# Kernel tuning notes

Hardware: AMD Instinct MI355X
Metric: run time of the kernel (lower is better)

## Reference

```python
import jax, jax.numpy as jnp
import numpy as np

B, N, C, H = 2, 2048, 1024, 16
D = C // H  # head_dim = 64
EPS = 1e-6


def _rope_freqs(n, d):
    inv_freq = 1.0 / (10000.0 ** (np.arange(0, d // 2, dtype=np.float32) * 2.0 / d))
    ang = np.arange(n, dtype=np.float32)[:, None] * inv_freq[None, :]  # [N, D/2]
    ang = np.concatenate([ang, ang], axis=-1)  # [N, D] (chunk-in-half convention)
    cos = jnp.asarray(np.cos(ang))[None, None]  # [1,1,N,D]
    sin = jnp.asarray(np.sin(ang))[None, None]
    return cos, sin


def setup_inputs() -> dict:
    key = jax.random.key(0)
    k1, k2, k3 = jax.random.split(key, 3)
    x = jax.random.normal(k1, (B, N, C), dtype=jnp.float32)
    w_qkv = jax.random.normal(k2, (3 * C, C), dtype=jnp.float32) * (C ** -0.5)
    w_proj = jax.random.normal(k3, (C, C), dtype=jnp.float32) * (C ** -0.5)
    b_proj = jnp.zeros((C,), dtype=jnp.float32)
    freqs_cos, freqs_sin = _rope_freqs(N, D)
    return {"x": x, "w_qkv": w_qkv, "w_proj": w_proj, "b_proj": b_proj,
            "freqs_cos": freqs_cos, "freqs_sin": freqs_sin}


def _layernorm(t):
    # affine-free LayerNorm over the last (head_dim) axis
    mu = jnp.mean(t, axis=-1, keepdims=True)
    var = jnp.var(t, axis=-1, keepdims=True)
    return (t - mu) * jax.lax.rsqrt(var + EPS)


def _rotate_half(t):
    t1, t2 = jnp.split(t, 2, axis=-1)
    return jnp.concatenate([-t2, t1], axis=-1)


def reference(x, w_qkv, w_proj, b_proj, freqs_cos, freqs_sin):
    b, n, c = x.shape
    qkv = jnp.einsum('bnc,kc->bnk', x, w_qkv)  # [B,N,3C]
    qkv = qkv.reshape(b, n, 3, H, D).transpose(2, 0, 3, 1, 4)  # [3,B,H,N,D]
    q, k, v = qkv[0], qkv[1], qkv[2]
    q = _layernorm(q)
    k = _layernorm(k)
    q = q * freqs_cos + _rotate_half(q) * freqs_sin
    k = k * freqs_cos + _rotate_half(k) * freqs_sin
    scale = D ** -0.5
    scores = jnp.einsum('bhqd,bhkd->bhqk', q, k) * scale  # [B,H,N,N]
    attn = jax.nn.softmax(scores, axis=-1)
    out = jnp.einsum('bhqk,bhkd->bhqd', attn, v)  # [B,H,N,D]
    out = out.transpose(0, 2, 1, 3).reshape(b, n, c)
    return jnp.einsum('bnc,oc->bno', out, w_proj) + b_proj
```

## Files before the change

### kernel.cpp

```cpp
#include <hip/hip_runtime.h>
#include <hip/hip_bf16.h>


typedef __bf16 bf16x8 __attribute__((ext_vector_type(8)));
typedef float f32x4 __attribute__((ext_vector_type(4)));
typedef float f32x16 __attribute__((ext_vector_type(16)));
typedef unsigned short us8 __attribute__((ext_vector_type(8)));
typedef unsigned short us4 __attribute__((ext_vector_type(4)));

static __device__ __forceinline__ unsigned short f2b(float f) {
  __hip_bfloat16 h = __float2bfloat16(f);
  return __builtin_bit_cast(unsigned short, h);
}
static __device__ __forceinline__ float b2f(unsigned short u) {
  __hip_bfloat16 h = __builtin_bit_cast(__hip_bfloat16, u);
  return __bfloat162float(h);
}

#if __has_builtin(__builtin_amdgcn_exp2f)
static __device__ __forceinline__ float fast_exp2(float x) { return __builtin_amdgcn_exp2f(x); }
#else
static __device__ __forceinline__ float fast_exp2(float x) { return exp2f(x); }
#endif

static __device__ __forceinline__ void async_copy16(void* lds, const void* g) {
  __builtin_amdgcn_global_load_lds(
      (const __attribute__((address_space(1))) void*)g,
      (__attribute__((address_space(3))) void*)lds, 16, 0, 0);
}

static __device__ __forceinline__ unsigned cvt_pk_bf16(float lo, float hi) {
  unsigned r;
  asm("v_cvt_pk_bf16_f32 %0, %1, %2" : "=v"(r) : "v"(lo), "v"(hi));
  return r;
}
static __device__ __forceinline__ void swap32(unsigned& x, unsigned& y) {
  asm("v_permlane32_swap_b32 %0, %1" : "+v"(x), "+v"(y));
}
static __device__ __forceinline__ float max3f(float a, float b, float c) {
  float d;
  asm("v_max3_f32 %0, %1, %2, %3" : "=v"(d) : "v"(a), "v"(b), "v"(c));
  return d;
}
static __device__ __forceinline__ float vmax16(const f32x16& v) {
  float a = max3f(v[0], v[1], v[2]);
  float b = max3f(v[3], v[4], v[5]);
  float c = max3f(v[6], v[7], v[8]);
  float d = max3f(v[9], v[10], v[11]);
  float e = max3f(v[12], v[13], v[14]);
  float x = max3f(a, b, c);
  float y = max3f(d, e, v[15]);
  return fmaxf(x, y);
}

__global__ __launch_bounds__(256) void cvt_bf16(
    const float* __restrict__ in, unsigned short* __restrict__ out, int n8) {
  int i = blockIdx.x * 256 + threadIdx.x;
  if (i >= n8) return;
  const float4* p = reinterpret_cast<const float4*>(in) + (size_t)i * 2;
  float4 a = p[0], b = p[1];
  us8 v;
  v[0] = f2b(a.x); v[1] = f2b(a.y); v[2] = f2b(a.z); v[3] = f2b(a.w);
  v[4] = f2b(b.x); v[5] = f2b(b.y); v[6] = f2b(b.z); v[7] = f2b(b.w);
  reinterpret_cast<us8*>(out)[i] = v;
}

__global__ __launch_bounds__(256, 2) void gemm_qkv(
    const unsigned short* __restrict__ A,
    const unsigned short* __restrict__ Bw,
    const float* __restrict__ fcos, const float* __restrict__ fsin,
    unsigned short* __restrict__ qo, unsigned short* __restrict__ ko,
    unsigned short* __restrict__ vt)
{
  __shared__ unsigned short a_sh[128 * 64];
  __shared__ unsigned short b_sh[128 * 64];
  const int tid = threadIdx.x;
  const int lane = tid & 63;
  const int w = tid >> 6;
  const int wr = w >> 1, wc = w & 1;
  const int l15 = lane & 15, l4 = lane >> 4;
  const int m0 = blockIdx.y * 128;
  const int n0 = blockIdx.x * 128;
  const int r8 = lane >> 3, c8 = lane & 7;
  const int K = 1024;

  f32x4 acc[4][4] = {};

  for (int k0 = 0; k0 < K; k0 += 64) {
#pragma unroll
    for (int p = 0; p < 8; ++p) {
      int s = p * 4 + w;
      if (s < 16) {
        int row = s * 8 + r8;
        async_copy16(&a_sh[s * 512],
                     &A[(size_t)(m0 + row) * K + k0 + ((c8 ^ (row & 7)) << 3)]);
      } else {
        int s2 = s - 16;
        int row = s2 * 8 + r8;
        async_copy16(&b_sh[s2 * 512],
                     &Bw[(size_t)(n0 + row) * K + k0 + ((c8 ^ (row & 7)) << 3)]);
      }
    }
    __syncthreads();
#pragma unroll
    for (int kk = 0; kk < 2; ++kk) {
      bf16x8 af[4], bfr[4];
#pragma unroll
      for (int mf = 0; mf < 4; ++mf) {
        int r = wr * 64 + mf * 16 + l15;
        af[mf] = *reinterpret_cast<const bf16x8*>(
            &a_sh[r * 64 + (((kk * 4 + l4) ^ (r & 7)) << 3)]);
      }
#pragma unroll
      for (int nf = 0; nf < 4; ++nf) {
        int r = wc * 64 + nf * 16 + l15;
        bfr[nf] = *reinterpret_cast<const bf16x8*>(
            &b_sh[r * 64 + (((kk * 4 + l4) ^ (r & 7)) << 3)]);
      }
#pragma unroll
      for (int mf = 0; mf < 4; ++mf)
#pragma unroll
        for (int nf = 0; nf < 4; ++nf)
          acc[mf][nf] = __builtin_amdgcn_mfma_f32_16x16x32_bf16(af[mf], bfr[nf], acc[mf][nf], 0, 0, 0);
    }
    __syncthreads();
  }

  const int colbase = n0 + wc * 64;
  const int three = colbase >> 10;
  const int hh = (colbase >> 6) & 15;
  const int b_ = m0 >> 11;
  const int nbase = (m0 & 2047) + wr * 64;
  unsigned short* ep = ((w < 2) ? a_sh : b_sh) + (w & 1) * 4096;
  const int cch = lane & 7, rb2 = lane >> 3;

  if (three < 2) {
    const float sc = three ? 1.f : 0.18033688011112042f;
#pragma unroll
    for (int mf = 0; mf < 4; ++mf) {
#pragma unroll
      for (int j = 0; j < 4; ++j) {
        float a0 = acc[mf][0][j], a1 = acc[mf][1][j];
        float a2 = acc[mf][2][j], a3 = acc[mf][3][j];
        float s1 = (a0 + a1) + (a2 + a3);
        float s2 = (a0 * a0 + a1 * a1) + (a2 * a2 + a3 * a3);
#pragma unroll
        for (int off = 8; off; off >>= 1) {
          s1 += __shfl_xor(s1, off);
          s2 += __shfl_xor(s2, off);
        }
        float mu = s1 * (1.f / 64.f);
        float inv = rsqrtf(s2 * (1.f / 64.f) - mu * mu + 1e-6f);
        int rloc = mf * 16 + l4 * 4 + j;
        int n = nbase + rloc;
        const float* cp = &fcos[(size_t)n * 64];
        const float* sp = &fsin[(size_t)n * 64];
#pragma unroll
        for (int nf = 0; nf < 4; ++nf) {
          int d = nf * 16 + l15;
          float tt = (acc[mf][nf][j] - mu) * inv;
          float tp = (acc[mf][nf ^ 2][j] - mu) * inv;
          float r = sc * (tt * cp[d] + ((nf < 2) ? -tp : tp) * sp[d]);
          ep[rloc * 64 + ((((d >> 3) ^ (rloc & 7)) << 3) | (d & 7))] = f2b(r);
        }
      }
    }
    unsigned short* dst =
        (three ? ko : qo) + (size_t)(b_ * 16 + hh) * 2048 * 64;
#pragma unroll
    for (int i = 0; i < 8; ++i) {
      int row = i * 8 + rb2;
      us8 vd = *reinterpret_cast<const us8*>(
          &ep[row * 64 + ((cch ^ (row & 7)) << 3)]);
      *reinterpret_cast<us8*>(&dst[(size_t)(nbase + row) * 64 + cch * 8]) = vd;
    }
  } else {
#pragma unroll
    for (int mf = 0; mf < 4; ++mf)
#pragma unroll
      for (int nf = 0; nf < 4; ++nf) {
        int d = nf * 16 + l15;
#pragma unroll
        for (int j = 0; j < 4; ++j) {
          int nl = mf * 16 + l4 * 4 + j;
          ep[d * 64 + ((((nl >> 3) ^ (d & 7)) << 3) | (nl & 7))] =
              f2b(acc[mf][nf][j]);
        }
      }
    unsigned short* dst = vt + (size_t)(b_ * 16 + hh) * 64 * 2048;
#pragma unroll
    for (int i = 0; i < 8; ++i) {
      int d = i * 8 + rb2;
      us8 vd = *reinterpret_cast<const us8*>(
          &ep[d * 64 + ((cch ^ (d & 7)) << 3)]);
      *reinterpret_cast<us8*>(&dst[(size_t)d * 2048 + nbase + cch * 8]) = vd;
    }
  }
}

__global__ __launch_bounds__(256, 2) void gemm_proj(
    const unsigned short* __restrict__ A, const unsigned short* __restrict__ Bw,
    const float* __restrict__ bias, float* __restrict__ Cout,
    int M, int Nn, int K) {
  __shared__ unsigned short a_sh[128 * 64];
  __shared__ unsigned short b_sh[128 * 64];
  const int tid = threadIdx.x;
  const int lane = tid & 63;
  const int w = tid >> 6;
  const int wr = w >> 1, wc = w & 1;
  const int l15 = lane & 15, l4 = lane >> 4;
  const int m0 = blockIdx.y * 128;
  const int n0 = blockIdx.x * 128;
  const int r8 = lane >> 3, c8 = lane & 7;

  f32x4 acc[4][4] = {};

  for (int k0 = 0; k0 < K; k0 += 64) {
#pragma unroll
    for (int p = 0; p < 8; ++p) {
      int s = p * 4 + w;
      if (s < 16) {
        int row = s * 8 + r8;
        async_copy16(&a_sh[s * 512],
                     &A[(size_t)(m0 + row) * K + k0 + ((c8 ^ (row & 7)) << 3)]);
      } else {
        int s2 = s - 16;
        int row = s2 * 8 + r8;
        async_copy16(&b_sh[s2 * 512],
                     &Bw[(size_t)(n0 + row) * K + k0 + ((c8 ^ (row & 7)) << 3)]);
      }
    }
    __syncthreads();
#pragma unroll
    for (int kk = 0; kk < 2; ++kk) {
      bf16x8 af[4], bfr[4];
#pragma unroll
      for (int mf = 0; mf < 4; ++mf) {
        int r = wr * 64 + mf * 16 + l15;
        af[mf] = *reinterpret_cast<const bf16x8*>(
            &a_sh[r * 64 + (((kk * 4 + l4) ^ (r & 7)) << 3)]);
      }
#pragma unroll
      for (int nf = 0; nf < 4; ++nf) {
        int r = wc * 64 + nf * 16 + l15;
        bfr[nf] = *reinterpret_cast<const bf16x8*>(
            &b_sh[r * 64 + (((kk * 4 + l4) ^ (r & 7)) << 3)]);
      }
#pragma unroll
      for (int mf = 0; mf < 4; ++mf)
#pragma unroll
        for (int nf = 0; nf < 4; ++nf)
          acc[mf][nf] = __builtin_amdgcn_mfma_f32_16x16x32_bf16(af[mf], bfr[nf], acc[mf][nf], 0, 0, 0);
    }
    __syncthreads();
  }
#pragma unroll
  for (int mf = 0; mf < 4; ++mf)
#pragma unroll
    for (int nf = 0; nf < 4; ++nf) {
      int col = n0 + wc * 64 + nf * 16 + l15;
#pragma unroll
      for (int j = 0; j < 4; ++j) {
        int row = m0 + wr * 64 + mf * 16 + l4 * 4 + j;
        Cout[(size_t)row * Nn + col] = acc[mf][nf][j] + bias[col];
      }
    }
}

__global__ __launch_bounds__(256, 4) void attn_kern(
    const unsigned short* __restrict__ Q,
    const unsigned short* __restrict__ Kk,
    const unsigned short* __restrict__ Vt,
    unsigned short* __restrict__ po,
    float* __restrict__ stats)
{
  __shared__ unsigned short k_sh[2][64 * 64];
  __shared__ unsigned short v_sh[2][64 * 64];
  const int tid = threadIdx.x;
  const int lane = tid & 63;
  const int w = tid >> 6;
  const int l31 = lane & 31;
  const int H = lane >> 5;
  const int bid = blockIdx.x;
  const int wid = (bid & 7) * 128 + (bid >> 3);
  const int split = wid & 1;
  const int qt = (wid >> 1) & 15;
  const int bh = wid >> 5;
  const int h = bh & 15, b = bh >> 4;
  const unsigned short* qb = Q + (size_t)bh * 2048 * 64;
  const unsigned short* kb = Kk + (size_t)bh * 2048 * 64;
  const unsigned short* vb = Vt + (size_t)bh * 64 * 2048;
  const int tok = qt * 128 + w * 32 + l31;
  const int kt0 = split * 16;

  bf16x8 qf[4];
#pragma unroll
  for (int c = 0; c < 4; ++c)
    qf[c] = *reinterpret_cast<const bf16x8*>(&qb[(size_t)tok * 64 + c * 16 + H * 8]);

  f32x16 oT[2] = {};
  float mr = -1e30f, lr = 0.f;

  const int r8 = lane >> 3, cc8 = lane & 7;
#define ATTN_STAGE(KT, BUF)                                                        \
  {                                                                                \
    _Pragma("unroll") for (int p = 0; p < 4; ++p) {                                \
      int sseg = p * 4 + w;                                                        \
      if (sseg < 8) {                                                              \
        int row = sseg * 8 + r8;                                                   \
        async_copy16(&k_sh[BUF][sseg * 512],                                       \
                     &kb[(size_t)((KT) * 64 + row) * 64 + ((cc8 ^ (row & 7)) << 3)]); \
      } else {                                                                     \
        int row = (sseg - 8) * 8 + r8;                                             \
        async_copy16(&v_sh[BUF][(sseg - 8) * 512],                                 \
                     &vb[(size_t)row * 2048 + (KT) * 64 + ((cc8 ^ (row & 7)) << 3)]); \
      }                                                                            \
    }                                                                              \
  }

  ATTN_STAGE(kt0, 0);
  __syncthreads();

  for (int kt = 0; kt < 16; ++kt) {
    const int cur = kt & 1;
    if (kt < 15) ATTN_STAGE(kt0 + kt + 1, cur ^ 1);

    f32x16 sT[2] = {};
#pragma unroll
    for (int c = 0; c < 4; ++c) {
      int ch0 = 2 * c + H;
#pragma unroll
      for (int t = 0; t < 2; ++t) {
        int r = t * 32 + l31;
        bf16x8 ka = *reinterpret_cast<const bf16x8*>(
            &k_sh[cur][r * 64 + ((ch0 ^ (r & 7)) << 3)]);
        sT[t] = __builtin_amdgcn_mfma_f32_32x32x16_bf16(ka, qf[c], sT[t], 0, 0, 0);
      }
    }
    float tmax = fmaxf(vmax16(sT[0]), vmax16(sT[1]));
    tmax = fmaxf(tmax, __shfl_xor(tmax, 32));
    if (__any(tmax > mr + 8.f)) {
      float mn = fmaxf(mr, tmax);
      float corr = fast_exp2(mr - mn);
      mr = mn;
      lr *= corr;
#pragma unroll
      for (int r = 0; r < 16; ++r) { oT[0][r] *= corr; oT[1][r] *= corr; }
    }
    float tsum = 0.f;
#pragma unroll
    for (int t = 0; t < 2; ++t)
#pragma unroll
      for (int r = 0; r < 16; ++r) {
        float p = fast_exp2(sT[t][r] - mr);
        sT[t][r] = p;
        tsum += p;
      }
    tsum += __shfl_xor(tsum, 32);
    lr += tsum;

    bf16x8 pB[4];
#pragma unroll
    for (int t = 0; t < 2; ++t)
#pragma unroll
      for (int half = 0; half < 2; ++half) {
        const int base = 8 * half;
        unsigned x0 = cvt_pk_bf16(sT[t][base + 0], sT[t][base + 1]);
        unsigned x1 = cvt_pk_bf16(sT[t][base + 2], sT[t][base + 3]);
        unsigned y0 = cvt_pk_bf16(sT[t][base + 4], sT[t][base + 5]);
        unsigned y1 = cvt_pk_bf16(sT[t][base + 6], sT[t][base + 7]);
        swap32(x0, y0);
        swap32(x1, y1);
        int4 packed = {(int)x0, (int)x1, (int)y0, (int)y1};
        pB[2 * t + half] = __builtin_bit_cast(bf16x8, packed);
      }
#pragma unroll
    for (int dt = 0; dt < 2; ++dt) {
      int r = dt * 32 + l31;
#pragma unroll
      for (int mi = 0; mi < 4; ++mi) {
        int ch = (mi * 2 + H) ^ (r & 7);
        bf16x8 va = *reinterpret_cast<const bf16x8*>(&v_sh[cur][r * 64 + (ch << 3)]);
        oT[dt] = __builtin_amdgcn_mfma_f32_32x32x16_bf16(va, pB[mi], oT[dt], 0, 0, 0);
      }
    }
    __syncthreads();
  }
  if (H == 0) {
    float2 st = {mr, lr};
    *reinterpret_cast<float2*>(
        &stats[(((size_t)split * 32 + bh) * 2048 + tok) * 2]) = st;
  }
  unsigned short* pd = po + (size_t)split * 4096 * 1024;
#pragma unroll
  for (int dt = 0; dt < 2; ++dt)
#pragma unroll
    for (int rb = 0; rb < 4; ++rb) {
      us4 ov;
#pragma unroll
      for (int j = 0; j < 4; ++j) ov[j] = f2b(oT[dt][rb * 4 + j]);
      *reinterpret_cast<us4*>(
          &pd[((size_t)b * 2048 + tok) * 1024 + h * 64 + 32 * dt + 8 * rb + 4 * H]) = ov;
    }
#undef ATTN_STAGE
}

__global__ __launch_bounds__(256) void attn_merge(
    const unsigned short* __restrict__ po,
    const float* __restrict__ stats,
    unsigned short* __restrict__ ao)
{
  int i = blockIdx.x * 256 + threadIdx.x;
  int row = i >> 8;
  int c4 = (i & 255) << 2;
  int b = row >> 11, tok = row & 2047, h = c4 >> 6;
  int bh = b * 16 + h;
  float2 s0 = *reinterpret_cast<const float2*>(&stats[((size_t)bh * 2048 + tok) * 2]);
  float2 s1 = *reinterpret_cast<const float2*>(
      &stats[(((size_t)32 + bh) * 2048 + tok) * 2]);
  float M = fmaxf(s0.x, s1.x);
  float w0 = fast_exp2(s0.x - M), w1 = fast_exp2(s1.x - M);
  float inv = 1.f / (s0.y * w0 + s1.y * w1);
  w0 *= inv; w1 *= inv;
  us4 a = *reinterpret_cast<const us4*>(&po[(size_t)i * 4]);
  us4 c = *reinterpret_cast<const us4*>(&po[(size_t)4096 * 1024 + i * 4]);
  us4 o;
#pragma unroll
  for (int j = 0; j < 4; ++j) o[j] = f2b(b2f(a[j]) * w0 + b2f(c[j]) * w1);
  *reinterpret_cast<us4*>(&ao[(size_t)i * 4]) = o;
}

extern "C" void kernel_launch(void* const* d_in, const int* in_sizes, int n_in,
                              void* d_out, int out_size, void* d_ws, size_t ws_size,
                              hipStream_t stream) {
  (void)in_sizes; (void)n_in; (void)out_size; (void)ws_size;
  const float* x      = (const float*)d_in[0];
  const float* w_qkv  = (const float*)d_in[1];
  const float* w_proj = (const float*)d_in[2];
  const float* b_proj = (const float*)d_in[3];
  const float* fcos   = (const float*)d_in[4];
  const float* fsin   = (const float*)d_in[5];
  float* out = (float*)d_out;
  char* ws = (char*)d_ws;

  unsigned short* x_bf     = (unsigned short*)(ws + 0);
  unsigned short* wqkv_bf  = (unsigned short*)(ws + 8388608);
  unsigned short* wproj_bf = (unsigned short*)(ws + 14680064);
  unsigned short* q_bf     = (unsigned short*)(ws + 16777216);
  unsigned short* k_bf     = (unsigned short*)(ws + 25165824);
  unsigned short* vt_bf    = (unsigned short*)(ws + 33554432);
  unsigned short* ao_bf    = (unsigned short*)(ws + 41943040);
  unsigned short* po_bf    = (unsigned short*)(ws + 50331648);
  float*          st_f     = (float*)(ws + 67108864);

  cvt_bf16<<<2048, 256, 0, stream>>>(x, x_bf, 4096 * 1024 / 8);
  cvt_bf16<<<1536, 256, 0, stream>>>(w_qkv, wqkv_bf, 3072 * 1024 / 8);
  cvt_bf16<<<512, 256, 0, stream>>>(w_proj, wproj_bf, 1024 * 1024 / 8);
  gemm_qkv<<<dim3(24, 32), 256, 0, stream>>>(x_bf, wqkv_bf, fcos, fsin,
                                             q_bf, k_bf, vt_bf);
  attn_kern<<<1024, 256, 0, stream>>>(q_bf, k_bf, vt_bf, po_bf, st_f);
  attn_merge<<<4096, 256, 0, stream>>>(po_bf, st_f, ao_bf);
  gemm_proj<<<dim3(8, 32), 256, 0, stream>>>(ao_bf, wproj_bf, b_proj, out,
                                             4096, 1024, 1024);
}
```

Baseline: 129.1 us.

## Drop split-KV attention and merge kernel, fuse bf16 conversions into one launch

```diff
diff --git a/kernel.cpp b/kernel.cpp
--- a/kernel.cpp
+++ b/kernel.cpp
@@ -53,19 +53,30 @@
   return fmaxf(x, y);
 }
 
-__global__ __launch_bounds__(256) void cvt_bf16(
-    const float* __restrict__ in, unsigned short* __restrict__ out, int n8) {
+__global__ __launch_bounds__(256) void cvt_all(
+    const float* __restrict__ x, const float* __restrict__ wqkv,
+    const float* __restrict__ wproj, unsigned short* __restrict__ x_bf,
+    unsigned short* __restrict__ wqkv_bf, unsigned short* __restrict__ wproj_bf) {
   int i = blockIdx.x * 256 + threadIdx.x;
-  if (i >= n8) return;
-  const float4* p = reinterpret_cast<const float4*>(in) + (size_t)i * 2;
+  const float* src;
+  unsigned short* dst;
+  int off;
+  if (i < 524288) {
+    src = x; dst = x_bf; off = i;
+  } else if (i < 917504) {
+    src = wqkv; dst = wqkv_bf; off = i - 524288;
+  } else {
+    src = wproj; dst = wproj_bf; off = i - 917504;
+  }
+  const float4* p = reinterpret_cast<const float4*>(src) + (size_t)off * 2;
   float4 a = p[0], b = p[1];
   us8 v;
   v[0] = f2b(a.x); v[1] = f2b(a.y); v[2] = f2b(a.z); v[3] = f2b(a.w);
   v[4] = f2b(b.x); v[5] = f2b(b.y); v[6] = f2b(b.z); v[7] = f2b(b.w);
-  reinterpret_cast<us8*>(out)[i] = v;
-}
-
-__global__ __launch_bounds__(256, 2) void gemm_qkv(
+  reinterpret_cast<us8*>(dst)[off] = v;
+}
+
+__global__ __launch_bounds__(256, 3) void gemm_qkv(
     const unsigned short* __restrict__ A,
     const unsigned short* __restrict__ Bw,
     const float* __restrict__ fcos, const float* __restrict__ fsin,
@@ -267,12 +278,11 @@
     }
 }
 
-__global__ __launch_bounds__(256, 4) void attn_kern(
+__global__ __launch_bounds__(256, 3) void attn_kern(
     const unsigned short* __restrict__ Q,
     const unsigned short* __restrict__ Kk,
     const unsigned short* __restrict__ Vt,
-    unsigned short* __restrict__ po,
-    float* __restrict__ stats)
+    unsigned short* __restrict__ O)
 {
   __shared__ unsigned short k_sh[2][64 * 64];
   __shared__ unsigned short v_sh[2][64 * 64];
@@ -282,16 +292,14 @@
   const int l31 = lane & 31;
   const int H = lane >> 5;
   const int bid = blockIdx.x;
-  const int wid = (bid & 7) * 128 + (bid >> 3);
-  const int split = wid & 1;
-  const int qt = (wid >> 1) & 15;
-  const int bh = wid >> 5;
+  const int wid = (bid & 7) * 64 + (bid >> 3);
+  const int qt = wid & 15;
+  const int bh = wid >> 4;
   const int h = bh & 15, b = bh >> 4;
   const unsigned short* qb = Q + (size_t)bh * 2048 * 64;
   const unsigned short* kb = Kk + (size_t)bh * 2048 * 64;
   const unsigned short* vb = Vt + (size_t)bh * 64 * 2048;
   const int tok = qt * 128 + w * 32 + l31;
-  const int kt0 = split * 16;
 
   bf16x8 qf[4];
 #pragma unroll
@@ -318,12 +326,12 @@
     }                                                                              \
   }
 
-  ATTN_STAGE(kt0, 0);
+  ATTN_STAGE(0, 0);
   __syncthreads();
 
-  for (int kt = 0; kt < 16; ++kt) {
+  for (int kt = 0; kt < 32; ++kt) {
     const int cur = kt & 1;
-    if (kt < 15) ATTN_STAGE(kt0 + kt + 1, cur ^ 1);
+    if (kt < 31) ATTN_STAGE(kt + 1, cur ^ 1);
 
     f32x16 sT[2] = {};
 #pragma unroll
@@ -386,48 +394,18 @@
     }
     __syncthreads();
   }
-  if (H == 0) {
-    float2 st = {mr, lr};
-    *reinterpret_cast<float2*>(
-        &stats[(((size_t)split * 32 + bh) * 2048 + tok) * 2]) = st;
-  }
-  unsigned short* pd = po + (size_t)split * 4096 * 1024;
+  float invl = 1.f / lr;
 #pragma unroll
   for (int dt = 0; dt < 2; ++dt)
 #pragma unroll
     for (int rb = 0; rb < 4; ++rb) {
       us4 ov;
 #pragma unroll
-      for (int j = 0; j < 4; ++j) ov[j] = f2b(oT[dt][rb * 4 + j]);
+      for (int j = 0; j < 4; ++j) ov[j] = f2b(oT[dt][rb * 4 + j] * invl);
       *reinterpret_cast<us4*>(
-          &pd[((size_t)b * 2048 + tok) * 1024 + h * 64 + 32 * dt + 8 * rb + 4 * H]) = ov;
+          &O[((size_t)b * 2048 + tok) * 1024 + h * 64 + 32 * dt + 8 * rb + 4 * H]) = ov;
     }
 #undef ATTN_STAGE
-}
-
-__global__ __launch_bounds__(256) void attn_merge(
-    const unsigned short* __restrict__ po,
-    const float* __restrict__ stats,
-    unsigned short* __restrict__ ao)
-{
-  int i = blockIdx.x * 256 + threadIdx.x;
-  int row = i >> 8;
-  int c4 = (i & 255) << 2;
-  int b = row >> 11, tok = row & 2047, h = c4 >> 6;
-  int bh = b * 16 + h;
-  float2 s0 = *reinterpret_cast<const float2*>(&stats[((size_t)bh * 2048 + tok) * 2]);
-  float2 s1 = *reinterpret_cast<const float2*>(
-      &stats[(((size_t)32 + bh) * 2048 + tok) * 2]);
-  float M = fmaxf(s0.x, s1.x);
-  float w0 = fast_exp2(s0.x - M), w1 = fast_exp2(s1.x - M);
-  float inv = 1.f / (s0.y * w0 + s1.y * w1);
-  w0 *= inv; w1 *= inv;
-  us4 a = *reinterpret_cast<const us4*>(&po[(size_t)i * 4]);
-  us4 c = *reinterpret_cast<const us4*>(&po[(size_t)4096 * 1024 + i * 4]);
-  us4 o;
-#pragma unroll
-  for (int j = 0; j < 4; ++j) o[j] = f2b(b2f(a[j]) * w0 + b2f(c[j]) * w1);
-  *reinterpret_cast<us4*>(&ao[(size_t)i * 4]) = o;
 }
 
 extern "C" void kernel_launch(void* const* d_in, const int* in_sizes, int n_in,
@@ -450,16 +428,11 @@
   unsigned short* k_bf     = (unsigned short*)(ws + 25165824);
   unsigned short* vt_bf    = (unsigned short*)(ws + 33554432);
   unsigned short* ao_bf    = (unsigned short*)(ws + 41943040);
-  unsigned short* po_bf    = (unsigned short*)(ws + 50331648);
-  float*          st_f     = (float*)(ws + 67108864);
-
-  cvt_bf16<<<2048, 256, 0, stream>>>(x, x_bf, 4096 * 1024 / 8);
-  cvt_bf16<<<1536, 256, 0, stream>>>(w_qkv, wqkv_bf, 3072 * 1024 / 8);
-  cvt_bf16<<<512, 256, 0, stream>>>(w_proj, wproj_bf, 1024 * 1024 / 8);
+
+  cvt_all<<<4096, 256, 0, stream>>>(x, w_qkv, w_proj, x_bf, wqkv_bf, wproj_bf);
   gemm_qkv<<<dim3(24, 32), 256, 0, stream>>>(x_bf, wqkv_bf, fcos, fsin,
                                              q_bf, k_bf, vt_bf);
-  attn_kern<<<1024, 256, 0, stream>>>(q_bf, k_bf, vt_bf, po_bf, st_f);
-  attn_merge<<<4096, 256, 0, stream>>>(po_bf, st_f, ao_bf);
+  attn_kern<<<512, 256, 0, stream>>>(q_bf, k_bf, vt_bf, ao_bf);
   gemm_proj<<<dim3(8, 32), 256, 0, stream>>>(ao_bf, wproj_bf, b_proj, out,
                                              4096, 1024, 1024);
 }
```

After: 118.8 us. 8.0% less time.
